# Performance work log

Measured on AMD Instinct MI355X. Metric: run time of the kernel, lower is better.

## Reference

```python
import math
import jax, jax.numpy as jnp
import numpy as np

B, T, C = 8, 1024, 768
H = 12
D = C // H  # 64


def setup_inputs() -> dict:
    key = jax.random.key(0)
    k1, k2, k3, k4, k5 = jax.random.split(key, 5)
    s = 0.02
    return {
        "x": jax.random.normal(k1, (B, T, C), dtype=jnp.float32),
        "w_qkv": jax.random.normal(k2, (C, 3 * C), dtype=jnp.float32) * s,
        "b_qkv": jax.random.normal(k3, (3 * C,), dtype=jnp.float32) * s,
        "w_proj": jax.random.normal(k4, (C, C), dtype=jnp.float32) * s,
        "b_proj": jax.random.normal(k5, (C,), dtype=jnp.float32) * s,
    }


def reference(x, w_qkv, b_qkv, w_proj, b_proj):
    b, t, c = x.shape
    qkv = x @ w_qkv + b_qkv                      # [B,T,3C]
    q, k, v = jnp.split(qkv, 3, axis=-1)
    # [B,T,C] -> [B,H,T,D]
    q = q.reshape(b, t, H, D).transpose(0, 2, 1, 3)
    k = k.reshape(b, t, H, D).transpose(0, 2, 1, 3)
    v = v.reshape(b, t, H, D).transpose(0, 2, 1, 3)
    scale = 1.0 / math.sqrt(D)
    att = jnp.einsum("bhqd,bhkd->bhqk", q, k) * scale   # [B,H,T,T]
    causal = jnp.tril(jnp.ones((t, t), dtype=bool))
    att = jnp.where(causal, att, -jnp.inf)
    att = jax.nn.softmax(att, axis=-1)
    y = jnp.einsum("bhqk,bhkd->bhqd", att, v)            # [B,H,T,D]
    y = y.transpose(0, 2, 1, 3).reshape(b, t, c)
    return y @ w_proj + b_proj
```

## Files before the change

kernel.cpp:

```cpp
#include <hip/hip_runtime.h>
#include <math.h>

#define B_ 8
#define T_ 1024
#define C_ 768
#define H_ 12
#define D_ 64

typedef __bf16 bf16x8 __attribute__((ext_vector_type(8)));
typedef float  f32x4  __attribute__((ext_vector_type(4)));
typedef unsigned short us8 __attribute__((ext_vector_type(8)));
typedef unsigned int   u32x4v __attribute__((ext_vector_type(4)));

typedef __attribute__((address_space(3))) void lds_void;
typedef __attribute__((address_space(1))) const void glb_void;

#define KSC 0.18033688011112043f

__device__ __forceinline__ unsigned short f2bf(float f) {
    unsigned int u = __float_as_uint(f);
    u += 0x7fffu + ((u >> 16) & 1u);
    return (unsigned short)(u >> 16);
}

__global__ __launch_bounds__(256)
void prep_w(const float* __restrict__ x,
            const float* __restrict__ w_qkv, const float* __restrict__ b_qkv,
            const float* __restrict__ w_proj,
            unsigned short* __restrict__ wqT, unsigned short* __restrict__ wpT,
            float* __restrict__ bqs, unsigned short* __restrict__ xb) {
    __shared__ unsigned short Ts[64][65];
    const int id  = blockIdx.x;
    const int tid = threadIdx.x;
    if (id >= 577) {
        const int xid = id - 577;
        const float4* xi = (const float4*)x;
        ushort4* xo = (ushort4*)xb;
#pragma unroll
        for (int it = 0; it < 6; it++) {
            const int idx = (xid * 6 + it) * 256 + tid;
            float4 v = xi[idx];
            ushort4 o;
            o.x = f2bf(v.x); o.y = f2bf(v.y); o.z = f2bf(v.z); o.w = f2bf(v.w);
            xo[idx] = o;
        }
        return;
    }
    if (id == 576) {
        for (int i = tid; i < 3 * C_; i += 256)
            bqs[i] = b_qkv[i] * (i < C_ ? KSC : 1.f);
        return;
    }
    const float* W; unsigned short* Wt; int N, nlim, t2;
    if (id < 432) { t2 = id;       W = w_qkv;  Wt = wqT; N = 3 * C_; nlim = C_; }
    else          { t2 = id - 432; W = w_proj; Wt = wpT; N = C_;     nlim = 0;  }
    const int ntiles = N / 64;
    const int n0 = (t2 % ntiles) * 64, k0 = (t2 / ntiles) * 64;
    for (int i = tid; i < 4096; i += 256) {
        int n = i & 63, k = i >> 6;
        float sc = (n0 + n < nlim) ? KSC : 1.f;
        Ts[n][k] = f2bf(W[(size_t)(k0 + k) * N + n0 + n] * sc);
    }
    __syncthreads();
    for (int i = tid; i < 4096; i += 256) {
        int k = i & 63, n = i >> 6;
        Wt[(size_t)(n0 + n) * 768 + k0 + k] = Ts[n][k];
    }
}

template<int OUT_BF16>
__global__ __launch_bounds__(256, 2)
void gemm_pipe(const unsigned short* __restrict__ A16,
               const unsigned short* __restrict__ Bt, const float* __restrict__ bias,
               void* __restrict__ Cout, int M, int N, int K) {
    __shared__ __align__(16) unsigned short As[2][8192];
    __shared__ __align__(16) unsigned short Bs[2][6144];

    const int tid  = threadIdx.x;
    const int lane = tid & 63;
    const int c    = lane & 15;
    const int quad = lane >> 4;
    const int wave = tid >> 6;
    const int wm   = (wave >> 1) * 64;
    const int wn   = (wave & 1) * 48;
    const int bm   = blockIdx.x * 128;
    const int bn   = blockIdx.y * 96;

    const unsigned short* aS[4];
    const unsigned short* bS[3];
#pragma unroll
    for (int p = 0; p < 4; p++) {
        const int Lp = p * 256 + tid;
        const int L  = Lp ^ ((Lp >> 3) & 7);
        aS[p] = A16 + (size_t)(bm + (L >> 3)) * K + (L & 7) * 8;
    }
#pragma unroll
    for (int p = 0; p < 3; p++) {
        const int Lp = p * 256 + tid;
        const int L  = Lp ^ ((Lp >> 3) & 7);
        bS[p] = Bt + (size_t)(bn + (L >> 3)) * K + (L & 7) * 8;
    }
    const int wb = (tid & 0xC0) * 8;

    int aoff[4][2], boff[3][2];
#pragma unroll
    for (int ks = 0; ks < 2; ks++) {
        const int kcA = (ks * 4 + quad) ^ (c & 7);
#pragma unroll
        for (int i = 0; i < 4; i++)
            aoff[i][ks] = ((wm + i * 16 + c) * 8 + kcA) * 8;
#pragma unroll
        for (int j = 0; j < 3; j++)
            boff[j][ks] = ((wn + j * 16 + c) * 8 + kcA) * 8;
    }

    f32x4 acc[4][3];
#pragma unroll
    for (int i = 0; i < 4; i++)
#pragma unroll
        for (int j = 0; j < 3; j++) acc[i][j] = (f32x4){0.f, 0.f, 0.f, 0.f};

#pragma unroll
    for (int p = 0; p < 4; p++) {
        __builtin_amdgcn_global_load_lds((glb_void*)aS[p],
            (lds_void*)(&As[0][0] + p * 2048 + wb), 16, 0, 0);
        aS[p] += 64;
    }
#pragma unroll
    for (int p = 0; p < 3; p++) {
        __builtin_amdgcn_global_load_lds((glb_void*)bS[p],
            (lds_void*)(&Bs[0][0] + p * 2048 + wb), 16, 0, 0);
        bS[p] += 64;
    }

    const int R = K >> 6;
    for (int r = 0; r < R; r++) {
        __syncthreads();

        if (r + 1 < R) {
#pragma unroll
            for (int p = 0; p < 4; p++) {
                __builtin_amdgcn_global_load_lds((glb_void*)aS[p],
                    (lds_void*)(&As[(r + 1) & 1][0] + p * 2048 + wb), 16, 0, 0);
                aS[p] += 64;
            }
#pragma unroll
            for (int p = 0; p < 3; p++) {
                __builtin_amdgcn_global_load_lds((glb_void*)bS[p],
                    (lds_void*)(&Bs[(r + 1) & 1][0] + p * 2048 + wb), 16, 0, 0);
                bS[p] += 64;
            }
        }

        const unsigned short* abuf = &As[r & 1][0];
        const unsigned short* bbuf = &Bs[r & 1][0];
#pragma unroll
        for (int ks = 0; ks < 2; ks++) {
            bf16x8 af[4], bfr[3];
#pragma unroll
            for (int i = 0; i < 4; i++)
                af[i] = __builtin_bit_cast(bf16x8, *(const us8*)&abuf[aoff[i][ks]]);
#pragma unroll
            for (int j = 0; j < 3; j++)
                bfr[j] = __builtin_bit_cast(bf16x8, *(const us8*)&bbuf[boff[j][ks]]);
#pragma unroll
            for (int i = 0; i < 4; i++)
#pragma unroll
                for (int j = 0; j < 3; j++)
                    acc[i][j] = __builtin_amdgcn_mfma_f32_16x16x32_bf16(af[i], bfr[j], acc[i][j], 0, 0, 0);
        }
    }

    float bs[3];
#pragma unroll
    for (int j = 0; j < 3; j++) bs[j] = bias[bn + wn + j * 16 + c];
#pragma unroll
    for (int i = 0; i < 4; i++) {
        const int gm = bm + wm + i * 16 + quad * 4;
#pragma unroll
        for (int r = 0; r < 4; r++) {
            const size_t ro = (size_t)(gm + r) * N;
#pragma unroll
            for (int j = 0; j < 3; j++) {
                const float v = acc[i][j][r] + bs[j];
                const int gn = bn + wn + j * 16 + c;
                if (OUT_BF16) ((unsigned short*)Cout)[ro + gn] = f2bf(v);
                else          ((float*)Cout)[ro + gn] = v;
            }
        }
    }
}

__device__ __forceinline__ int sigmaK(int k) {
    return 16 * (2 * (k >> 5) + ((k >> 2) & 1)) + 4 * ((k >> 3) & 3) + (k & 3);
}

__global__ __launch_bounds__(256, 3)
void attn_mfma(const unsigned short* __restrict__ qkv, unsigned short* __restrict__ y) {
    __shared__ __align__(16) unsigned short Ks[64 * 72];
    __shared__ __align__(16) unsigned int   Vt[64 * 36];

    const int tid  = threadIdx.x;
    const int wave = tid >> 6;
    const int lane = tid & 63;
    const int c    = lane & 15;
    const int quad = lane >> 4;

    const int id = blockIdx.x;
    const int p  = (id >> 3) & 7;
    const int bh = (id >> 6) * 8 + (id & 7);
    const int b  = bh / H_;
    const int h  = bh - b * H_;

    const int qts[2] = {p, 15 - p};
    const int q0s[2] = {p * 64, (15 - p) * 64};

    const int RS = 3 * C_;
    const unsigned short* kbase = qkv + (size_t)b * T_ * RS + C_ + h * D_;
    const unsigned short* vbase = qkv + (size_t)b * T_ * RS + 2 * C_ + h * D_;

    const u32x4v onesu = {0x3F803F80u, 0x3F803F80u, 0x3F803F80u, 0x3F803F80u};
    const bf16x8 onesf = __builtin_bit_cast(bf16x8, onesu);

    bf16x8 qf[2][2];
#pragma unroll
    for (int t = 0; t < 2; t++) {
        const unsigned short* qrow =
            qkv + ((size_t)(b * T_ + q0s[t] + wave * 16 + c)) * RS + h * D_ + quad * 8;
        qf[t][0] = __builtin_bit_cast(bf16x8, *(const us8*)qrow);
        qf[t][1] = __builtin_bit_cast(bf16x8, *(const us8*)(qrow + 32));
    }

    const int kr0 = tid >> 3, kc0 = tid & 7;
    const int sK0 = sigmaK(kr0) * 72 + kc0 * 8;
    const int sK1 = sigmaK(kr0 + 32) * 72 + kc0 * 8;
    const int dg  = tid >> 4, kp0 = tid & 15;

    us8 kA, kB;
    ushort4 vA0, vB0, vA1, vB1;
    {
        kA = *(const us8*)(kbase + (size_t)kr0 * RS + kc0 * 8);
        kB = *(const us8*)(kbase + (size_t)(kr0 + 32) * RS + kc0 * 8);
        const unsigned short* p0 = vbase + (size_t)(2 * kp0) * RS + dg * 4;
        vA0 = *(const ushort4*)p0;  vB0 = *(const ushort4*)(p0 + RS);
        const unsigned short* p1 = vbase + (size_t)(2 * (kp0 + 16)) * RS + dg * 4;
        vA1 = *(const ushort4*)p1;  vB1 = *(const ushort4*)(p1 + RS);
    }

    f32x4 Oa[2][4];
    f32x4 Ol[2];
#pragma unroll
    for (int t = 0; t < 2; t++) {
        Ol[t] = (f32x4){0.f, 0.f, 0.f, 0.f};
#pragma unroll
        for (int d = 0; d < 4; d++) Oa[t][d] = (f32x4){0.f, 0.f, 0.f, 0.f};
    }

    const int ktEnd = qts[1];
    for (int kt = 0; kt <= ktEnd; kt++) {
        __syncthreads();
        *(us8*)&Ks[sK0] = kA;
        *(us8*)&Ks[sK1] = kB;
        {
            unsigned int* v0 = &Vt[(dg * 4) * 36 + kp0];
            v0[0]   = vA0.x | ((unsigned)vB0.x << 16);
            v0[36]  = vA0.y | ((unsigned)vB0.y << 16);
            v0[72]  = vA0.z | ((unsigned)vB0.z << 16);
            v0[108] = vA0.w | ((unsigned)vB0.w << 16);
            unsigned int* v1 = v0 + 16;
            v1[0]   = vA1.x | ((unsigned)vB1.x << 16);
            v1[36]  = vA1.y | ((unsigned)vB1.y << 16);
            v1[72]  = vA1.z | ((unsigned)vB1.z << 16);
            v1[108] = vA1.w | ((unsigned)vB1.w << 16);
        }
        __syncthreads();

        if (kt < ktEnd) {
            const unsigned short* kp = kbase + (size_t)((kt + 1) * 64) * RS;
            kA = *(const us8*)(kp + (size_t)kr0 * RS + kc0 * 8);
            kB = *(const us8*)(kp + (size_t)(kr0 + 32) * RS + kc0 * 8);
            const unsigned short* vp = vbase + (size_t)((kt + 1) * 64) * RS;
            const unsigned short* p0 = vp + (size_t)(2 * kp0) * RS + dg * 4;
            vA0 = *(const ushort4*)p0;  vB0 = *(const ushort4*)(p0 + RS);
            const unsigned short* p1 = vp + (size_t)(2 * (kp0 + 16)) * RS + dg * 4;
            vA1 = *(const ushort4*)p1;  vB1 = *(const ushort4*)(p1 + RS);
        }

        bf16x8 kf[4][2];
#pragma unroll
        for (int nb = 0; nb < 4; nb++) {
#pragma unroll
            for (int ks = 0; ks < 2; ks++)
                kf[nb][ks] = __builtin_bit_cast(bf16x8,
                    *(const us8*)&Ks[(nb * 16 + c) * 72 + quad * 8 + ks * 32]);
        }

#pragma unroll
        for (int t = 0; t < 2; t++) {
            if (kt > qts[t]) continue;
            const bool diag = (kt == qts[t]);
            const bool doHi = !diag || (wave >= 2);
            const int nbmax = diag ? ((wave >= 2) ? 3 : 1) : 3;

            f32x4 sv[4];
            __builtin_amdgcn_s_setprio(1);
#pragma unroll
            for (int nb = 0; nb < 4; nb++) {
                if (nb <= nbmax) {
                    f32x4 z = (f32x4){0.f, 0.f, 0.f, 0.f};
                    z = __builtin_amdgcn_mfma_f32_16x16x32_bf16(kf[nb][0], qf[t][0], z, 0, 0, 0);
                    sv[nb] = __builtin_amdgcn_mfma_f32_16x16x32_bf16(kf[nb][1], qf[t][1], z, 0, 0, 0);
                }
            }
            __builtin_amdgcn_s_setprio(0);
            if (diag) {
                const int qloc = wave * 16 + c;
#pragma unroll
                for (int nb = 0; nb < 4; nb++) {
                    if (nb <= nbmax) {
                        const int kb = 32 * (nb >> 1) + 4 * (nb & 1) + 8 * quad;
#pragma unroll
                        for (int r = 0; r < 4; r++)
                            if (kb + r > qloc) sv[nb][r] = -INFINITY;
                    }
                }
            }

            unsigned int pd[4][2];
#pragma unroll
            for (int nb = 0; nb < 4; nb++) {
                if (nb <= nbmax) {
                    float p0 = __builtin_amdgcn_exp2f(sv[nb][0]);
                    float p1 = __builtin_amdgcn_exp2f(sv[nb][1]);
                    float p2 = __builtin_amdgcn_exp2f(sv[nb][2]);
                    float p3 = __builtin_amdgcn_exp2f(sv[nb][3]);
                    unsigned u0 = __float_as_uint(p0) + 0x8000u;
                    unsigned u1 = __float_as_uint(p1) + 0x8000u;
                    unsigned u2 = __float_as_uint(p2) + 0x8000u;
                    unsigned u3 = __float_as_uint(p3) + 0x8000u;
                    pd[nb][0] = (u0 >> 16) | (u1 & 0xffff0000u);
                    pd[nb][1] = (u2 >> 16) | (u3 & 0xffff0000u);
                } else {
                    pd[nb][0] = 0u; pd[nb][1] = 0u;
                }
            }

            bf16x8 ap0 = __builtin_bit_cast(bf16x8,
                (u32x4v){pd[0][0], pd[0][1], pd[1][0], pd[1][1]});
            bf16x8 ap1 = __builtin_bit_cast(bf16x8,
                (u32x4v){pd[2][0], pd[2][1], pd[3][0], pd[3][1]});

            __builtin_amdgcn_s_setprio(1);
            Ol[t] = __builtin_amdgcn_mfma_f32_16x16x32_bf16(ap0, onesf, Ol[t], 0, 0, 0);
            if (doHi)
                Ol[t] = __builtin_amdgcn_mfma_f32_16x16x32_bf16(ap1, onesf, Ol[t], 0, 0, 0);

#pragma unroll
            for (int dd = 0; dd < 4; dd++) {
                const unsigned int* vrow = &Vt[(dd * 16 + c) * 36 + quad * 4];
                bf16x8 vb0 = __builtin_bit_cast(bf16x8, *(const u32x4v*)vrow);
                Oa[t][dd] = __builtin_amdgcn_mfma_f32_16x16x32_bf16(ap0, vb0, Oa[t][dd], 0, 0, 0);
                if (doHi) {
                    bf16x8 vb1 = __builtin_bit_cast(bf16x8, *(const u32x4v*)(vrow + 16));
                    Oa[t][dd] = __builtin_amdgcn_mfma_f32_16x16x32_bf16(ap1, vb1, Oa[t][dd], 0, 0, 0);
                }
            }
            __builtin_amdgcn_s_setprio(0);
        }
    }

#pragma unroll
    for (int t = 0; t < 2; t++) {
        unsigned short* yrow =
            y + ((size_t)(b * T_ + q0s[t] + wave * 16)) * C_ + h * D_;
#pragma unroll
        for (int r = 0; r < 4; r++) {
            float inv = 1.f / Ol[t][r];
#pragma unroll
            for (int dd = 0; dd < 4; dd++)
                yrow[(size_t)(quad * 4 + r) * C_ + dd * 16 + c] = f2bf(Oa[t][dd][r] * inv);
        }
    }
}

extern "C" void kernel_launch(void* const* d_in, const int* in_sizes, int n_in,
                              void* d_out, int out_size, void* d_ws, size_t ws_size,
                              hipStream_t stream) {
    const float* x      = (const float*)d_in[0];
    const float* w_qkv  = (const float*)d_in[1];
    const float* b_qkv  = (const float*)d_in[2];
    const float* w_proj = (const float*)d_in[3];
    const float* b_proj = (const float*)d_in[4];
    float* out = (float*)d_out;

    unsigned short* wqT  = (unsigned short*)d_ws;
    unsigned short* wpT  = wqT  + (size_t)3 * C_ * C_;
    unsigned short* qkvb = wpT  + (size_t)C_ * C_;
    unsigned short* yb   = qkvb + (size_t)B_ * T_ * 3 * C_;
    float*          bqs  = (float*)(yb + (size_t)B_ * T_ * C_);

    unsigned short* xb = yb;

    prep_w<<<1601, 256, 0, stream>>>(x, w_qkv, b_qkv, w_proj, wqT, wpT, bqs, xb);

    gemm_pipe<1><<<dim3(B_ * T_ / 128, 3 * C_ / 96), 256, 0, stream>>>(
        xb, wqT, bqs, qkvb, B_ * T_, 3 * C_, C_);

    attn_mfma<<<8 * B_ * H_, 256, 0, stream>>>(qkvb, yb);

    gemm_pipe<0><<<dim3(B_ * T_ / 128, C_ / 96), 256, 0, stream>>>(
        yb, wpT, b_proj, out, B_ * T_, C_, C_);
}
```

Before: 175.9 us.

## Load GEMM B fragments directly into registers instead of staging through LDS

The GEMM kernel no longer stages the B (weight) tile in shared memory. Each lane loads its B fragments from global memory straight into double-buffered registers, prefetching the next k-step while the current one computes, and the k-loop is unrolled by two to alternate the buffers. This halves-plus the LDS footprint so launch bounds ask for 3 blocks per CU instead of 2, and it removes the LDS writes and reads for B. The cost is more global/L2 traffic, because B data is no longer shared across waves (two waves share each B column range), plus extra register pressure. The unroll-by-two assumes R (K/64 = 12) is even.

```diff
diff --git a/kernel.cpp b/kernel.cpp
--- a/kernel.cpp
+++ b/kernel.cpp
@@ -69,12 +69,11 @@
 }
 
 template<int OUT_BF16>
-__global__ __launch_bounds__(256, 2)
-void gemm_pipe(const unsigned short* __restrict__ A16,
+__global__ __launch_bounds__(256, 3)
+void gemm_breg(const unsigned short* __restrict__ A16,
                const unsigned short* __restrict__ Bt, const float* __restrict__ bias,
                void* __restrict__ Cout, int M, int N, int K) {
     __shared__ __align__(16) unsigned short As[2][8192];
-    __shared__ __align__(16) unsigned short Bs[2][6144];
 
     const int tid  = threadIdx.x;
     const int lane = tid & 63;
@@ -87,38 +86,32 @@
     const int bn   = blockIdx.y * 96;
 
     const unsigned short* aS[4];
-    const unsigned short* bS[3];
 #pragma unroll
     for (int p = 0; p < 4; p++) {
         const int Lp = p * 256 + tid;
         const int L  = Lp ^ ((Lp >> 3) & 7);
         aS[p] = A16 + (size_t)(bm + (L >> 3)) * K + (L & 7) * 8;
     }
-#pragma unroll
-    for (int p = 0; p < 3; p++) {
-        const int Lp = p * 256 + tid;
-        const int L  = Lp ^ ((Lp >> 3) & 7);
-        bS[p] = Bt + (size_t)(bn + (L >> 3)) * K + (L & 7) * 8;
-    }
     const int wb = (tid & 0xC0) * 8;
 
-    int aoff[4][2], boff[3][2];
+    int aoff[4][2];
 #pragma unroll
     for (int ks = 0; ks < 2; ks++) {
         const int kcA = (ks * 4 + quad) ^ (c & 7);
 #pragma unroll
         for (int i = 0; i < 4; i++)
             aoff[i][ks] = ((wm + i * 16 + c) * 8 + kcA) * 8;
-#pragma unroll
-        for (int j = 0; j < 3; j++)
-            boff[j][ks] = ((wn + j * 16 + c) * 8 + kcA) * 8;
-    }
+    }
+
+    const unsigned short* bP = Bt + (size_t)(bn + wn + c) * K + quad * 8;
 
     f32x4 acc[4][3];
 #pragma unroll
     for (int i = 0; i < 4; i++)
 #pragma unroll
         for (int j = 0; j < 3; j++) acc[i][j] = (f32x4){0.f, 0.f, 0.f, 0.f};
+
+    us8 b0[3][2], b1[3][2];
 
 #pragma unroll
     for (int p = 0; p < 4; p++) {
@@ -127,49 +120,53 @@
         aS[p] += 64;
     }
 #pragma unroll
-    for (int p = 0; p < 3; p++) {
-        __builtin_amdgcn_global_load_lds((glb_void*)bS[p],
-            (lds_void*)(&Bs[0][0] + p * 2048 + wb), 16, 0, 0);
-        bS[p] += 64;
-    }
+    for (int j = 0; j < 3; j++)
+#pragma unroll
+        for (int ks = 0; ks < 2; ks++)
+            b0[j][ks] = *(const us8*)(bP + (size_t)j * 16 * K + ks * 32);
 
     const int R = K >> 6;
-    for (int r = 0; r < R; r++) {
-        __syncthreads();
-
-        if (r + 1 < R) {
-#pragma unroll
-            for (int p = 0; p < 4; p++) {
-                __builtin_amdgcn_global_load_lds((glb_void*)aS[p],
-                    (lds_void*)(&As[(r + 1) & 1][0] + p * 2048 + wb), 16, 0, 0);
-                aS[p] += 64;
-            }
-#pragma unroll
-            for (int p = 0; p < 3; p++) {
-                __builtin_amdgcn_global_load_lds((glb_void*)bS[p],
-                    (lds_void*)(&Bs[(r + 1) & 1][0] + p * 2048 + wb), 16, 0, 0);
-                bS[p] += 64;
-            }
-        }
-
-        const unsigned short* abuf = &As[r & 1][0];
-        const unsigned short* bbuf = &Bs[r & 1][0];
-#pragma unroll
-        for (int ks = 0; ks < 2; ks++) {
-            bf16x8 af[4], bfr[3];
-#pragma unroll
-            for (int i = 0; i < 4; i++)
-                af[i] = __builtin_bit_cast(bf16x8, *(const us8*)&abuf[aoff[i][ks]]);
-#pragma unroll
-            for (int j = 0; j < 3; j++)
-                bfr[j] = __builtin_bit_cast(bf16x8, *(const us8*)&bbuf[boff[j][ks]]);
-#pragma unroll
-            for (int i = 0; i < 4; i++)
-#pragma unroll
-                for (int j = 0; j < 3; j++)
-                    acc[i][j] = __builtin_amdgcn_mfma_f32_16x16x32_bf16(af[i], bfr[j], acc[i][j], 0, 0, 0);
-        }
-    }
+
+#define GEMM_ROUND(CUR, NXT, RR)                                               \
+    __syncthreads();                                                           \
+    if ((RR) + 1 < R) {                                                        \
+        _Pragma("unroll")                                                      \
+        for (int p = 0; p < 4; p++) {                                          \
+            __builtin_amdgcn_global_load_lds((glb_void*)aS[p],                 \
+                (lds_void*)(&As[((RR) + 1) & 1][0] + p * 2048 + wb), 16, 0, 0);\
+            aS[p] += 64;                                                       \
+        }                                                                      \
+        _Pragma("unroll")                                                      \
+        for (int j = 0; j < 3; j++) {                                          \
+            _Pragma("unroll")                                                  \
+            for (int ks = 0; ks < 2; ks++)                                     \
+                NXT[j][ks] = *(const us8*)(bP + (size_t)j * 16 * K +           \
+                                           ((RR) + 1) * 64 + ks * 32);         \
+        }                                                                      \
+    }                                                                          \
+    {                                                                          \
+        const unsigned short* abuf = &As[(RR) & 1][0];                         \
+        _Pragma("unroll")                                                      \
+        for (int ks = 0; ks < 2; ks++) {                                       \
+            bf16x8 af[4];                                                      \
+            _Pragma("unroll")                                                  \
+            for (int i = 0; i < 4; i++)                                        \
+                af[i] = __builtin_bit_cast(bf16x8, *(const us8*)&abuf[aoff[i][ks]]); \
+            _Pragma("unroll")                                                  \
+            for (int i = 0; i < 4; i++)                                        \
+                _Pragma("unroll")                                              \
+                for (int j = 0; j < 3; j++)                                    \
+                    acc[i][j] = __builtin_amdgcn_mfma_f32_16x16x32_bf16(       \
+                        af[i], __builtin_bit_cast(bf16x8, CUR[j][ks]),         \
+                        acc[i][j], 0, 0, 0);                                   \
+        }                                                                      \
+    }
+
+    for (int r = 0; r < R; r += 2) {
+        GEMM_ROUND(b0, b1, r)
+        GEMM_ROUND(b1, b0, r + 1)
+    }
+#undef GEMM_ROUND
 
     float bs[3];
 #pragma unroll
@@ -403,11 +400,11 @@
 
     prep_w<<<1601, 256, 0, stream>>>(x, w_qkv, b_qkv, w_proj, wqT, wpT, bqs, xb);
 
-    gemm_pipe<1><<<dim3(B_ * T_ / 128, 3 * C_ / 96), 256, 0, stream>>>(
+    gemm_breg<1><<<dim3(B_ * T_ / 128, 3 * C_ / 96), 256, 0, stream>>>(
         xb, wqT, bqs, qkvb, B_ * T_, 3 * C_, C_);
 
     attn_mfma<<<8 * B_ * H_, 256, 0, stream>>>(qkvb, yb);
 
-    gemm_pipe<0><<<dim3(B_ * T_ / 128, C_ / 96), 256, 0, stream>>>(
+    gemm_breg<0><<<dim3(B_ * T_ / 128, C_ / 96), 256, 0, stream>>>(
         yb, wpT, b_proj, out, B_ * T_, C_, C_);
 }
```

Measured after the change: 208.8 us. 1.19x slower.

## Double-buffer K/V tiles in LDS to use one barrier per iteration

Applied to the files above, without the earlier changes.

The attention kernel's K and V shared-memory tiles become double-buffered. Each iteration writes the next tile into the alternate buffer and issues global loads two tiles ahead, with a single barrier at the end of the loop instead of two. This removes a synchronisation point and overlaps LDS staging with compute. It doubles LDS use per block, which may limit occupancy at the 3-blocks-per-CU launch bound, and it adds register pressure.

```diff
diff --git a/kernel.cpp b/kernel.cpp
--- a/kernel.cpp
+++ b/kernel.cpp
@@ -197,8 +197,8 @@
 
 __global__ __launch_bounds__(256, 3)
 void attn_mfma(const unsigned short* __restrict__ qkv, unsigned short* __restrict__ y) {
-    __shared__ __align__(16) unsigned short Ks[64 * 72];
-    __shared__ __align__(16) unsigned int   Vt[64 * 36];
+    __shared__ __align__(16) unsigned short Ks[2][64 * 72];
+    __shared__ __align__(16) unsigned int   Vt[2][64 * 36];
 
     const int tid  = threadIdx.x;
     const int wave = tid >> 6;
@@ -238,6 +238,7 @@
 
     us8 kA, kB;
     ushort4 vA0, vB0, vA1, vB1;
+
     {
         kA = *(const us8*)(kbase + (size_t)kr0 * RS + kc0 * 8);
         kB = *(const us8*)(kbase + (size_t)(kr0 + 32) * RS + kc0 * 8);
@@ -246,6 +247,31 @@
         const unsigned short* p1 = vbase + (size_t)(2 * (kp0 + 16)) * RS + dg * 4;
         vA1 = *(const ushort4*)p1;  vB1 = *(const ushort4*)(p1 + RS);
     }
+    *(us8*)&Ks[0][sK0] = kA;
+    *(us8*)&Ks[0][sK1] = kB;
+    {
+        unsigned int* v0 = &Vt[0][(dg * 4) * 36 + kp0];
+        v0[0]   = vA0.x | ((unsigned)vB0.x << 16);
+        v0[36]  = vA0.y | ((unsigned)vB0.y << 16);
+        v0[72]  = vA0.z | ((unsigned)vB0.z << 16);
+        v0[108] = vA0.w | ((unsigned)vB0.w << 16);
+        unsigned int* v1 = v0 + 16;
+        v1[0]   = vA1.x | ((unsigned)vB1.x << 16);
+        v1[36]  = vA1.y | ((unsigned)vB1.y << 16);
+        v1[72]  = vA1.z | ((unsigned)vB1.z << 16);
+        v1[108] = vA1.w | ((unsigned)vB1.w << 16);
+    }
+    {
+        const unsigned short* kp = kbase + (size_t)64 * RS;
+        kA = *(const us8*)(kp + (size_t)kr0 * RS + kc0 * 8);
+        kB = *(const us8*)(kp + (size_t)(kr0 + 32) * RS + kc0 * 8);
+        const unsigned short* vp = vbase + (size_t)64 * RS;
+        const unsigned short* p0 = vp + (size_t)(2 * kp0) * RS + dg * 4;
+        vA0 = *(const ushort4*)p0;  vB0 = *(const ushort4*)(p0 + RS);
+        const unsigned short* p1 = vp + (size_t)(2 * (kp0 + 16)) * RS + dg * 4;
+        vA1 = *(const ushort4*)p1;  vB1 = *(const ushort4*)(p1 + RS);
+    }
+    __syncthreads();
 
     f32x4 Oa[2][4];
     f32x4 Ol[2];
@@ -258,32 +284,33 @@
 
     const int ktEnd = qts[1];
     for (int kt = 0; kt <= ktEnd; kt++) {
-        __syncthreads();
-        *(us8*)&Ks[sK0] = kA;
-        *(us8*)&Ks[sK1] = kB;
-        {
-            unsigned int* v0 = &Vt[(dg * 4) * 36 + kp0];
-            v0[0]   = vA0.x | ((unsigned)vB0.x << 16);
-            v0[36]  = vA0.y | ((unsigned)vB0.y << 16);
-            v0[72]  = vA0.z | ((unsigned)vB0.z << 16);
-            v0[108] = vA0.w | ((unsigned)vB0.w << 16);
-            unsigned int* v1 = v0 + 16;
-            v1[0]   = vA1.x | ((unsigned)vB1.x << 16);
-            v1[36]  = vA1.y | ((unsigned)vB1.y << 16);
-            v1[72]  = vA1.z | ((unsigned)vB1.z << 16);
-            v1[108] = vA1.w | ((unsigned)vB1.w << 16);
-        }
-        __syncthreads();
+        const int cur = kt & 1, nxt = cur ^ 1;
 
         if (kt < ktEnd) {
-            const unsigned short* kp = kbase + (size_t)((kt + 1) * 64) * RS;
-            kA = *(const us8*)(kp + (size_t)kr0 * RS + kc0 * 8);
-            kB = *(const us8*)(kp + (size_t)(kr0 + 32) * RS + kc0 * 8);
-            const unsigned short* vp = vbase + (size_t)((kt + 1) * 64) * RS;
-            const unsigned short* p0 = vp + (size_t)(2 * kp0) * RS + dg * 4;
-            vA0 = *(const ushort4*)p0;  vB0 = *(const ushort4*)(p0 + RS);
-            const unsigned short* p1 = vp + (size_t)(2 * (kp0 + 16)) * RS + dg * 4;
-            vA1 = *(const ushort4*)p1;  vB1 = *(const ushort4*)(p1 + RS);
+            *(us8*)&Ks[nxt][sK0] = kA;
+            *(us8*)&Ks[nxt][sK1] = kB;
+            {
+                unsigned int* v0 = &Vt[nxt][(dg * 4) * 36 + kp0];
+                v0[0]   = vA0.x | ((unsigned)vB0.x << 16);
+                v0[36]  = vA0.y | ((unsigned)vB0.y << 16);
+                v0[72]  = vA0.z | ((unsigned)vB0.z << 16);
+                v0[108] = vA0.w | ((unsigned)vB0.w << 16);
+                unsigned int* v1 = v0 + 16;
+                v1[0]   = vA1.x | ((unsigned)vB1.x << 16);
+                v1[36]  = vA1.y | ((unsigned)vB1.y << 16);
+                v1[72]  = vA1.z | ((unsigned)vB1.z << 16);
+                v1[108] = vA1.w | ((unsigned)vB1.w << 16);
+            }
+            if (kt + 2 <= ktEnd) {
+                const unsigned short* kp = kbase + (size_t)((kt + 2) * 64) * RS;
+                kA = *(const us8*)(kp + (size_t)kr0 * RS + kc0 * 8);
+                kB = *(const us8*)(kp + (size_t)(kr0 + 32) * RS + kc0 * 8);
+                const unsigned short* vp = vbase + (size_t)((kt + 2) * 64) * RS;
+                const unsigned short* p0 = vp + (size_t)(2 * kp0) * RS + dg * 4;
+                vA0 = *(const ushort4*)p0;  vB0 = *(const ushort4*)(p0 + RS);
+                const unsigned short* p1 = vp + (size_t)(2 * (kp0 + 16)) * RS + dg * 4;
+                vA1 = *(const ushort4*)p1;  vB1 = *(const ushort4*)(p1 + RS);
+            }
         }
 
         bf16x8 kf[4][2];
@@ -292,7 +319,7 @@
 #pragma unroll
             for (int ks = 0; ks < 2; ks++)
                 kf[nb][ks] = __builtin_bit_cast(bf16x8,
-                    *(const us8*)&Ks[(nb * 16 + c) * 72 + quad * 8 + ks * 32]);
+                    *(const us8*)&Ks[cur][(nb * 16 + c) * 72 + quad * 8 + ks * 32]);
         }
 
 #pragma unroll
@@ -357,7 +384,7 @@
 
 #pragma unroll
             for (int dd = 0; dd < 4; dd++) {
-                const unsigned int* vrow = &Vt[(dd * 16 + c) * 36 + quad * 4];
+                const unsigned int* vrow = &Vt[cur][(dd * 16 + c) * 36 + quad * 4];
                 bf16x8 vb0 = __builtin_bit_cast(bf16x8, *(const u32x4v*)vrow);
                 Oa[t][dd] = __builtin_amdgcn_mfma_f32_16x16x32_bf16(ap0, vb0, Oa[t][dd], 0, 0, 0);
                 if (doHi) {
@@ -367,6 +394,8 @@
             }
             __builtin_amdgcn_s_setprio(0);
         }
+
+        __syncthreads();
     }
 
 #pragma unroll
```

Result: no change. 177.5 us (+0.9%).

## Widen GEMM to 256x96 tiles with 512 threads and deeper async prefetch

Applied to the files above, without the earlier changes.

The GEMM kernel now uses 512-thread blocks covering 256 rows, so the B tile is shared by twice as many rows. The pipeline issues two stages ahead and waits with explicit vmcnt counts and raw s_barrier instead of __syncthreads. MFMA sections are raised in priority with s_setprio. The intent is to cut B-tile reload traffic and hide more load latency. The cost is half as many blocks, one block per CU, more LDS, and waitcnt accounting that has to stay correct for the unequal per-wave load counts.

```diff
diff --git a/kernel.cpp b/kernel.cpp
--- a/kernel.cpp
+++ b/kernel.cpp
@@ -69,11 +69,11 @@
 }
 
 template<int OUT_BF16>
-__global__ __launch_bounds__(256, 2)
-void gemm_pipe(const unsigned short* __restrict__ A16,
+__global__ __launch_bounds__(512, 1)
+void gemm_wide(const unsigned short* __restrict__ A16,
                const unsigned short* __restrict__ Bt, const float* __restrict__ bias,
                void* __restrict__ Cout, int M, int N, int K) {
-    __shared__ __align__(16) unsigned short As[2][8192];
+    __shared__ __align__(16) unsigned short As[2][16384];
     __shared__ __align__(16) unsigned short Bs[2][6144];
 
     const int tid  = threadIdx.x;
@@ -83,24 +83,29 @@
     const int wave = tid >> 6;
     const int wm   = (wave >> 1) * 64;
     const int wn   = (wave & 1) * 48;
-    const int bm   = blockIdx.x * 128;
+    const int bm   = blockIdx.x * 256;
     const int bn   = blockIdx.y * 96;
 
     const unsigned short* aS[4];
-    const unsigned short* bS[3];
 #pragma unroll
     for (int p = 0; p < 4; p++) {
-        const int Lp = p * 256 + tid;
+        const int Lp = p * 512 + tid;
         const int L  = Lp ^ ((Lp >> 3) & 7);
         aS[p] = A16 + (size_t)(bm + (L >> 3)) * K + (L & 7) * 8;
     }
-#pragma unroll
-    for (int p = 0; p < 3; p++) {
-        const int Lp = p * 256 + tid;
+    const unsigned short* bS0;
+    const unsigned short* bS1;
+    {
+        const int Lp = tid;
         const int L  = Lp ^ ((Lp >> 3) & 7);
-        bS[p] = Bt + (size_t)(bn + (L >> 3)) * K + (L & 7) * 8;
-    }
-    const int wb = (tid & 0xC0) * 8;
+        bS0 = Bt + (size_t)(bn + (L >> 3)) * K + (L & 7) * 8;
+    }
+    {
+        const int Lp = 512 + (tid & 255);
+        const int L  = Lp ^ ((Lp >> 3) & 7);
+        bS1 = Bt + (size_t)(bn + (L >> 3)) * K + (L & 7) * 8;
+    }
+    const int wbA = (tid & 0x1C0) * 8;
 
     int aoff[4][2], boff[3][2];
 #pragma unroll
@@ -120,56 +125,64 @@
 #pragma unroll
         for (int j = 0; j < 3; j++) acc[i][j] = (f32x4){0.f, 0.f, 0.f, 0.f};
 
-#pragma unroll
-    for (int p = 0; p < 4; p++) {
-        __builtin_amdgcn_global_load_lds((glb_void*)aS[p],
-            (lds_void*)(&As[0][0] + p * 2048 + wb), 16, 0, 0);
-        aS[p] += 64;
-    }
-#pragma unroll
-    for (int p = 0; p < 3; p++) {
-        __builtin_amdgcn_global_load_lds((glb_void*)bS[p],
-            (lds_void*)(&Bs[0][0] + p * 2048 + wb), 16, 0, 0);
-        bS[p] += 64;
-    }
+#define STAGE(BUF)                                                             \
+    {                                                                          \
+        _Pragma("unroll")                                                      \
+        for (int p = 0; p < 4; p++) {                                          \
+            __builtin_amdgcn_global_load_lds((glb_void*)aS[p],                 \
+                (lds_void*)(&As[BUF][0] + p * 4096 + wbA), 16, 0, 0);          \
+            aS[p] += 64;                                                       \
+        }                                                                      \
+        __builtin_amdgcn_global_load_lds((glb_void*)bS0,                       \
+            (lds_void*)(&Bs[BUF][0] + wbA), 16, 0, 0);                         \
+        bS0 += 64;                                                             \
+        if (wave < 4) {                                                        \
+            __builtin_amdgcn_global_load_lds((glb_void*)bS1,                   \
+                (lds_void*)(&Bs[BUF][0] + 4096 + wbA), 16, 0, 0);              \
+            bS1 += 64;                                                         \
+        }                                                                      \
+    }
+
+    STAGE(0)
+    STAGE(1)
 
     const int R = K >> 6;
-    for (int r = 0; r < R; r++) {
-        __syncthreads();
-
-        if (r + 1 < R) {
-#pragma unroll
-            for (int p = 0; p < 4; p++) {
-                __builtin_amdgcn_global_load_lds((glb_void*)aS[p],
-                    (lds_void*)(&As[(r + 1) & 1][0] + p * 2048 + wb), 16, 0, 0);
-                aS[p] += 64;
-            }
-#pragma unroll
-            for (int p = 0; p < 3; p++) {
-                __builtin_amdgcn_global_load_lds((glb_void*)bS[p],
-                    (lds_void*)(&Bs[(r + 1) & 1][0] + p * 2048 + wb), 16, 0, 0);
-                bS[p] += 64;
-            }
-        }
-
-        const unsigned short* abuf = &As[r & 1][0];
-        const unsigned short* bbuf = &Bs[r & 1][0];
+    int cur = 0;
+    for (int t = 0; t < R; t++) {
+        if (t + 1 < R) {
+            if (wave < 4) asm volatile("s_waitcnt vmcnt(6)" ::: "memory");
+            else          asm volatile("s_waitcnt vmcnt(5)" ::: "memory");
+        } else {
+            asm volatile("s_waitcnt vmcnt(0)" ::: "memory");
+        }
+        asm volatile("s_barrier" ::: "memory");
+
+        const unsigned short* ab = &As[cur][0];
+        const unsigned short* bb = &Bs[cur][0];
 #pragma unroll
         for (int ks = 0; ks < 2; ks++) {
             bf16x8 af[4], bfr[3];
 #pragma unroll
             for (int i = 0; i < 4; i++)
-                af[i] = __builtin_bit_cast(bf16x8, *(const us8*)&abuf[aoff[i][ks]]);
+                af[i] = __builtin_bit_cast(bf16x8, *(const us8*)&ab[aoff[i][ks]]);
 #pragma unroll
             for (int j = 0; j < 3; j++)
-                bfr[j] = __builtin_bit_cast(bf16x8, *(const us8*)&bbuf[boff[j][ks]]);
+                bfr[j] = __builtin_bit_cast(bf16x8, *(const us8*)&bb[boff[j][ks]]);
+            __builtin_amdgcn_s_setprio(1);
 #pragma unroll
             for (int i = 0; i < 4; i++)
 #pragma unroll
                 for (int j = 0; j < 3; j++)
                     acc[i][j] = __builtin_amdgcn_mfma_f32_16x16x32_bf16(af[i], bfr[j], acc[i][j], 0, 0, 0);
-        }
-    }
+            __builtin_amdgcn_s_setprio(0);
+        }
+
+        asm volatile("s_barrier" ::: "memory");
+
+        if (t + 2 < R) STAGE(cur)
+        cur ^= 1;
+    }
+#undef STAGE
 
     float bs[3];
 #pragma unroll
@@ -403,11 +416,11 @@
 
     prep_w<<<1601, 256, 0, stream>>>(x, w_qkv, b_qkv, w_proj, wqT, wpT, bqs, xb);
 
-    gemm_pipe<1><<<dim3(B_ * T_ / 128, 3 * C_ / 96), 256, 0, stream>>>(
+    gemm_wide<1><<<dim3(B_ * T_ / 256, 3 * C_ / 96), 512, 0, stream>>>(
         xb, wqT, bqs, qkvb, B_ * T_, 3 * C_, C_);
 
     attn_mfma<<<8 * B_ * H_, 256, 0, stream>>>(qkvb, yb);
 
-    gemm_pipe<0><<<dim3(B_ * T_ / 128, C_ / 96), 256, 0, stream>>>(
+    gemm_wide<0><<<dim3(B_ * T_ / 256, C_ / 96), 512, 0, stream>>>(
         yb, wpT, b_proj, out, B_ * T_, C_, C_);
 }
```

Result: slower. 186.2 us (+5.8%).
